# Kernel tuning notes

Hardware: AMD Instinct MI355X
Metric: run time of the kernel (lower is better)

Reference implementation:

```python
import jax, jax.numpy as jnp
import numpy as np

N, C, V, T = 16, 32, 512, 64
H, EMB, D = 4, 64, 16
OUT_C = 64
BN_EPS = 1e-5


def setup_inputs() -> dict:
    key = jax.random.key(0)
    ks = jax.random.split(key, 12)
    x = jax.random.normal(ks[0], (N, C, V, T), dtype=jnp.float32)
    t_in = jax.random.uniform(ks[1], (N, T), dtype=jnp.float32)
    # random-walk-like supports; scaled so chained nconv hops stay O(1)
    A0 = jax.random.normal(ks[2], (V, V), dtype=jnp.float32) * (V ** -0.5)
    A1 = jax.random.normal(ks[3], (V, V), dtype=jnp.float32) * (V ** -0.5)
    A2 = jax.random.normal(ks[4], (V, V), dtype=jnp.float32) * (V ** -0.5)
    factors = jax.random.normal(ks[5], (H,), dtype=jnp.float32) * 0.1
    Wq = jax.random.normal(ks[6], (H, EMB, D), dtype=jnp.float32) * (EMB ** -0.5)
    Wk = jax.random.normal(ks[7], (H, EMB, D), dtype=jnp.float32) * (EMB ** -0.5)
    GC_IN = 7 * C  # (order*support_len + 1) * in_channels
    W_out = jax.random.normal(ks[8], (OUT_C, GC_IN), dtype=jnp.float32) * (GC_IN ** -0.5)
    b_out = jnp.zeros((OUT_C,), dtype=jnp.float32)
    W_res = jax.random.normal(ks[9], (OUT_C, C), dtype=jnp.float32) * (C ** -0.5)
    b_res = jnp.zeros((OUT_C,), dtype=jnp.float32)
    bn_gamma = jnp.ones((OUT_C,), dtype=jnp.float32)
    bn_beta = jnp.zeros((OUT_C,), dtype=jnp.float32)
    bn_mean = jnp.zeros((OUT_C,), dtype=jnp.float32)
    bn_var = jnp.ones((OUT_C,), dtype=jnp.float32)
    alpha = jnp.full((1,), 0.25, dtype=jnp.float32)  # PReLU init
    return dict(x=x, t_in=t_in, A0=A0, A1=A1, A2=A2, factors=factors,
                Wq=Wq, Wk=Wk, W_out=W_out, b_out=b_out,
                W_res=W_res, b_res=b_res, bn_gamma=bn_gamma, bn_beta=bn_beta,
                bn_mean=bn_mean, bn_var=bn_var, alpha=alpha)


def reference(x, t_in, A0, A1, A2, factors, Wq, Wk, W_out, b_out,
              W_res, b_res, bn_gamma, bn_beta, bn_mean, bn_var, alpha):
    # --- learnEmbedding, all heads at once: emb[b,h,t,f] ---
    div = jnp.arange(0, EMB, 2, dtype=x.dtype)           # [EMB/2]
    div_term = jnp.exp(div[None, :] * factors[:, None])  # [H, EMB/2]
    phase = jnp.einsum('bt,hf->bhtf', t_in, div_term)    # [N,H,T,EMB/2]
    emb = jnp.concatenate([jnp.sin(phase), jnp.cos(phase)], axis=-1)  # [N,H,T,EMB]
    # --- ATT per head (t_out=None => q_emb == k_emb) ---
    q = jnp.einsum('bhtf,hfd->bhtd', emb, Wq)
    k = jnp.einsum('bhtf,hfd->bhtd', emb, Wk)
    att = jax.nn.softmax(jnp.einsum('bhtd,bhpd->bhtp', q, k) / (D ** 0.5), axis=-1)  # [N,H,T,T]
    # --- temporal mixing, summed over heads (matches per-head += loop) ---
    xt = jnp.einsum('ncvt,nhpt->ncvp', x, att)           # [N,C,V,T]
    # --- gcn: diffusion over 3 supports, order 2 ---
    outs = [xt]
    for A in (A0, A1, A2):
        x1 = jnp.einsum('ncvl,vw->ncwl', xt, A)
        x2 = jnp.einsum('ncvl,vw->ncwl', x1, A)
        outs.extend([x1, x2])
    h = jnp.concatenate(outs, axis=1)                    # [N,7C,V,T]
    # --- 1x1 output projection ---
    y = jnp.einsum('ncvt,oc->novt', h, W_out) + b_out[None, :, None, None]
    # --- residual branch: 1x1 conv + BatchNorm (eval) ---
    r = jnp.einsum('ncvt,oc->novt', x, W_res) + b_res[None, :, None, None]
    r = (r - bn_mean[None, :, None, None]) * jax.lax.rsqrt(bn_var + BN_EPS)[None, :, None, None]
    r = r * bn_gamma[None, :, None, None] + bn_beta[None, :, None, None]
    # --- residual add + PReLU (dropout is identity in eval) ---
    out = y + r
    out = jnp.where(out > 0, out, alpha[0] * out)
    return out
```

## Files before the change

kernel.cpp:

```cpp
#include <hip/hip_runtime.h>

namespace {
constexpr int N_ = 16, C_ = 32, V_ = 512, T_ = 64;
constexpr int H_ = 4, D_ = 16, OC_ = 64;
constexpr int EMB_ = 64;
constexpr int GCIN_ = 7 * C_;
constexpr int TV_ = T_ * V_;
}

typedef _Float16 f16x8 __attribute__((ext_vector_type(8)));
typedef _Float16 f16x4 __attribute__((ext_vector_type(4)));
typedef float f32x4 __attribute__((ext_vector_type(4)));

__global__ __launch_bounds__(64) void att_kernel(
    const float* __restrict__ t_in, const float* __restrict__ factors,
    const float* __restrict__ Wq, const float* __restrict__ Wk,
    float* __restrict__ att)
{
    const int n = blockIdx.x >> 2;
    const int h = blockIdx.x & 3;
    const int t = threadIdx.x;

    __shared__ float wq_l[EMB_][D_];
    __shared__ float wk_l[EMB_][D_];
    __shared__ float k_l[T_][D_ + 1];

#pragma unroll
    for (int d = 0; d < D_; ++d) {
        wq_l[t][d] = Wq[(h * EMB_ + t) * D_ + d];
        wk_l[t][d] = Wk[(h * EMB_ + t) * D_ + d];
    }
    __syncthreads();

    const float tv = t_in[n * T_ + t];
    const float fh = factors[h];
    float emb[EMB_];
#pragma unroll
    for (int j = 0; j < 32; ++j) {
        float dt = __expf((float)(2 * j) * fh);
        float ph = tv * dt;
        float s, c;
        __sincosf(ph, &s, &c);
        emb[j] = s;
        emb[j + 32] = c;
    }

    float q[D_];
#pragma unroll
    for (int d = 0; d < D_; ++d) {
        float aq = 0.f, ak = 0.f;
#pragma unroll
        for (int f = 0; f < EMB_; ++f) {
            aq += emb[f] * wq_l[f][d];
            ak += emb[f] * wk_l[f][d];
        }
        q[d] = aq;
        k_l[t][d] = ak;
    }
    __syncthreads();

    float L[T_];
    float m = -1e30f;
#pragma unroll
    for (int j = 0; j < T_; ++j) {
        float a = 0.f;
#pragma unroll
        for (int d = 0; d < D_; ++d) a += q[d] * k_l[j][d];
        a *= 0.25f;
        L[j] = a;
        m = fmaxf(m, a);
    }
    float ssum = 0.f;
#pragma unroll
    for (int j = 0; j < T_; ++j) {
        float e = __expf(L[j] - m);
        L[j] = e;
        ssum += e;
    }
    const float inv = 1.f / ssum;
    float* arow = att + (((size_t)(n * H_ + h) * T_ + t) * T_);
#pragma unroll
    for (int j = 0; j < T_; ++j) arow[j] = L[j] * inv;
}

__global__ __launch_bounds__(256) void sred_kernel(
    const float* __restrict__ att, float* __restrict__ S)
{
    int g = blockIdx.x * 256 + threadIdx.x;
    if (g >= N_ * T_ * T_) return;
    int n = g / (T_ * T_);
    int ij = g - n * (T_ * T_);
    float a = 0.f;
#pragma unroll
    for (int h = 0; h < H_; ++h) a += att[(size_t)(n * H_ + h) * (T_ * T_) + ij];
    S[g] = a;
}

__global__ __launch_bounds__(256) void prepAt_kernel(
    const float* __restrict__ A0, const float* __restrict__ A1,
    const float* __restrict__ A2, _Float16* __restrict__ At16)
{
    const int s = blockIdx.z;
    const float* A = (s == 0) ? A0 : ((s == 1) ? A1 : A2);
    const int v0 = blockIdx.y * 32, w0 = blockIdx.x * 32;
    const int tid = threadIdx.x;
    __shared__ float sT[32][33];
#pragma unroll
    for (int k = 0; k < 4; ++k) {
        int lin = k * 256 + tid;
        int i = lin >> 5, w = lin & 31;
        sT[i][w] = A[(size_t)(v0 + i) * V_ + w0 + w];
    }
    __syncthreads();
#pragma unroll
    for (int k = 0; k < 4; ++k) {
        int lin = k * 256 + tid;
        int j = lin >> 5, i = lin & 31;
        At16[(size_t)s * V_ * V_ + (size_t)(w0 + j) * V_ + v0 + i] = (_Float16)sT[i][j];
    }
}

__global__ __launch_bounds__(256) void prepxT_kernel(
    const float* __restrict__ x, _Float16* __restrict__ xT, int n0)
{
    const int b = blockIdx.z;
    const int v0 = blockIdx.x * 32;
    const int t0 = blockIdx.y * 32;
    const int tid = threadIdx.x;
    __shared__ float sT[32][33];
    const float* xb = x + ((size_t)(n0 * C_) + b) * (size_t)(V_ * T_);
    {
        int vi = tid >> 3, tq = tid & 7;
        *(float4*)&sT[vi][tq * 4] = *(const float4*)&xb[(size_t)(v0 + vi) * T_ + t0 + tq * 4];
    }
    __syncthreads();
    {
        int tj = tid >> 3, vq = tid & 7;
        f16x4 o4;
        o4[0] = (_Float16)sT[vq * 4 + 0][tj];
        o4[1] = (_Float16)sT[vq * 4 + 1][tj];
        o4[2] = (_Float16)sT[vq * 4 + 2][tj];
        o4[3] = (_Float16)sT[vq * 4 + 3][tj];
        *(f16x4*)&xT[(size_t)b * TV_ + (size_t)(t0 + tj) * V_ + v0 + vq * 4] = o4;
    }
}

__global__ __launch_bounds__(256) void prepW_kernel(
    const float* __restrict__ W_out, const float* __restrict__ b_out,
    const float* __restrict__ W_res, const float* __restrict__ b_res,
    const float* __restrict__ gamma, const float* __restrict__ beta,
    const float* __restrict__ mean, const float* __restrict__ var,
    _Float16* __restrict__ Wcat, float* __restrict__ bias)
{
    const int tid = threadIdx.x;
    const int o = tid & 63;
    const int kb = tid >> 6;
    const float rs = gamma[o] * rsqrtf(var[o] + 1e-5f);
    for (int kk = 0; kk < 64; ++kk) {
        int k = kb * 64 + kk;
        float w = (k < GCIN_) ? W_out[o * GCIN_ + k] : rs * W_res[o * C_ + (k - GCIN_)];
        Wcat[o * 256 + k] = (_Float16)w;
    }
    if (tid < 64) bias[tid] = b_out[tid] + beta[tid] + rs * (b_res[tid] - mean[tid]);
}

__global__ __launch_bounds__(256) void xtT_kernel(
    const float* __restrict__ x, const float* __restrict__ S,
    _Float16* __restrict__ XT, int n0)
{
    const int b = blockIdx.y;
    const int n = n0 + b / C_;
    const int lane = threadIdx.x & 63;
    const int wav = threadIdx.x >> 6;
    const int vbase = blockIdx.x * 256 + wav * 64;
    const int row16 = lane & 15;
    const int kg = lane >> 4;

    const float* Sn = S + (size_t)n * (T_ * T_);
    const float* xb = x + ((size_t)(n0 * C_) + b) * (V_ * T_);

    f32x4 acc[4][4];
#pragma unroll
    for (int i = 0; i < 4; ++i)
#pragma unroll
        for (int j = 0; j < 4; ++j) acc[i][j] = (f32x4){0.f, 0.f, 0.f, 0.f};

#pragma unroll
    for (int ks = 0; ks < 2; ++ks) {
        f16x8 a[4], bf[4];
#pragma unroll
        for (int mt = 0; mt < 4; ++mt) {
            const float* p = xb + (size_t)(vbase + mt * 16 + row16) * T_ + ks * 32 + kg * 8;
            float4 u = *(const float4*)p;
            float4 w = *(const float4*)(p + 4);
            f16x8 t8;
            t8[0] = (_Float16)u.x; t8[1] = (_Float16)u.y; t8[2] = (_Float16)u.z; t8[3] = (_Float16)u.w;
            t8[4] = (_Float16)w.x; t8[5] = (_Float16)w.y; t8[6] = (_Float16)w.z; t8[7] = (_Float16)w.w;
            a[mt] = t8;
        }
#pragma unroll
        for (int nt = 0; nt < 4; ++nt) {
            const float* p = Sn + (size_t)(nt * 16 + row16) * T_ + ks * 32 + kg * 8;
            float4 u = *(const float4*)p;
            float4 w = *(const float4*)(p + 4);
            f16x8 t8;
            t8[0] = (_Float16)u.x; t8[1] = (_Float16)u.y; t8[2] = (_Float16)u.z; t8[3] = (_Float16)u.w;
            t8[4] = (_Float16)w.x; t8[5] = (_Float16)w.y; t8[6] = (_Float16)w.z; t8[7] = (_Float16)w.w;
            bf[nt] = t8;
        }
#pragma unroll
        for (int nt = 0; nt < 4; ++nt)
#pragma unroll
            for (int mt = 0; mt < 4; ++mt)
                acc[mt][nt] = __builtin_amdgcn_mfma_f32_16x16x32_f16(a[mt], bf[nt], acc[mt][nt], 0, 0, 0);
    }

    _Float16* Yb = XT + (size_t)b * TV_;
#pragma unroll
    for (int mt = 0; mt < 4; ++mt)
#pragma unroll
        for (int nt = 0; nt < 4; ++nt) {
            int p = nt * 16 + row16;
            int v = vbase + mt * 16 + kg * 4;
            f16x4 h;
            h[0] = (_Float16)acc[mt][nt][0];
            h[1] = (_Float16)acc[mt][nt][1];
            h[2] = (_Float16)acc[mt][nt][2];
            h[3] = (_Float16)acc[mt][nt][3];
            *(f16x4*)&Yb[(size_t)p * V_ + v] = h;
        }
}

__global__ __launch_bounds__(512) void hopf_kernel(
    const _Float16* __restrict__ At16, _Float16* __restrict__ Hb,
    unsigned long long ASZ)
{
    const int b = blockIdx.x;
    const int s = blockIdx.y;
    const int tid = threadIdx.x;
    const int lane = tid & 63;
    const int wav = tid >> 6;
    const int wbase = wav * 64;
    const int row16 = lane & 15;
    const int kg = lane >> 4;

    __shared__ _Float16 x1s[T_ * V_];

    const _Float16* At = At16 + (size_t)s * V_ * V_;
    const _Float16* Xb = Hb + (size_t)b * TV_;
    _Float16* Y1 = Hb + (size_t)(1 + 2 * s) * ASZ + (size_t)b * TV_;
    _Float16* Y2 = Hb + (size_t)(2 + 2 * s) * ASZ + (size_t)b * TV_;

    const _Float16* ax = At + (size_t)(wbase + row16) * V_ + kg * 8;

    f32x4 acc[4][4];
    f16x8 aC[4], bC[4], aN[4], bN[4];

#pragma unroll
    for (int k = 0; k < 8; ++k) {
        int lin = k * 512 + tid;
        int t = lin >> 6;
        int v8 = (lin & 63) << 3;
        f16x8 val = *(const f16x8*)&Xb[(size_t)t * V_ + v8];
        int byte = (t * V_ + v8) * 2;
        *(f16x8*)((char*)x1s + (byte ^ ((t & 7) << 4))) = val;
    }
    __syncthreads();

#pragma unroll
    for (int i = 0; i < 4; ++i)
#pragma unroll
        for (int j = 0; j < 4; ++j) acc[i][j] = (f32x4){0.f, 0.f, 0.f, 0.f};

#pragma unroll
    for (int i = 0; i < 4; ++i) {
        aC[i] = *(const f16x8*)(ax + (size_t)i * 16 * V_);
        int t = i * 16 + row16;
        int byte = (t * V_ + kg * 8) * 2;
        bC[i] = *(const f16x8*)((const char*)x1s + (byte ^ ((t & 7) << 4)));
    }
#pragma unroll
    for (int v0 = 0; v0 < V_; v0 += 32) {
        if (v0 + 32 < V_) {
#pragma unroll
            for (int i = 0; i < 4; ++i) {
                aN[i] = *(const f16x8*)(ax + (size_t)i * 16 * V_ + v0 + 32);
                int t = i * 16 + row16;
                int byte = (t * V_ + v0 + 32 + kg * 8) * 2;
                bN[i] = *(const f16x8*)((const char*)x1s + (byte ^ ((t & 7) << 4)));
            }
        }
#pragma unroll
        for (int nt = 0; nt < 4; ++nt)
#pragma unroll
            for (int mt = 0; mt < 4; ++mt)
                acc[mt][nt] = __builtin_amdgcn_mfma_f32_16x16x32_f16(aC[mt], bC[nt], acc[mt][nt], 0, 0, 0);
#pragma unroll
        for (int i = 0; i < 4; ++i) { aC[i] = aN[i]; bC[i] = bN[i]; }
    }
    __syncthreads();

#pragma unroll
    for (int mt = 0; mt < 4; ++mt)
#pragma unroll
        for (int nt = 0; nt < 4; ++nt) {
            int t = nt * 16 + row16;
            int w = wbase + mt * 16 + kg * 4;
            f16x4 h;
            h[0] = (_Float16)acc[mt][nt][0];
            h[1] = (_Float16)acc[mt][nt][1];
            h[2] = (_Float16)acc[mt][nt][2];
            h[3] = (_Float16)acc[mt][nt][3];
            int byte = (t * V_ + w) * 2;
            *(f16x4*)((char*)x1s + (byte ^ ((t & 7) << 4))) = h;
        }
    __syncthreads();

#pragma unroll
    for (int k = 0; k < 8; ++k) {
        int lin = k * 512 + tid;
        int t = lin >> 6;
        int v8 = (lin & 63) << 3;
        int byte = (t * V_ + v8) * 2;
        f16x8 val = *(const f16x8*)((const char*)x1s + (byte ^ ((t & 7) << 4)));
        *(f16x8*)&Y1[(size_t)t * V_ + v8] = val;
    }

#pragma unroll
    for (int i = 0; i < 4; ++i)
#pragma unroll
        for (int j = 0; j < 4; ++j) acc[i][j] = (f32x4){0.f, 0.f, 0.f, 0.f};

#pragma unroll
    for (int i = 0; i < 4; ++i) {
        aC[i] = *(const f16x8*)(ax + (size_t)i * 16 * V_);
        int t = i * 16 + row16;
        int byte = (t * V_ + kg * 8) * 2;
        bC[i] = *(const f16x8*)((const char*)x1s + (byte ^ ((t & 7) << 4)));
    }
#pragma unroll
    for (int v0 = 0; v0 < V_; v0 += 32) {
        if (v0 + 32 < V_) {
#pragma unroll
            for (int i = 0; i < 4; ++i) {
                aN[i] = *(const f16x8*)(ax + (size_t)i * 16 * V_ + v0 + 32);
                int t = i * 16 + row16;
                int byte = (t * V_ + v0 + 32 + kg * 8) * 2;
                bN[i] = *(const f16x8*)((const char*)x1s + (byte ^ ((t & 7) << 4)));
            }
        }
#pragma unroll
        for (int nt = 0; nt < 4; ++nt)
#pragma unroll
            for (int mt = 0; mt < 4; ++mt)
                acc[mt][nt] = __builtin_amdgcn_mfma_f32_16x16x32_f16(aC[mt], bC[nt], acc[mt][nt], 0, 0, 0);
#pragma unroll
        for (int i = 0; i < 4; ++i) { aC[i] = aN[i]; bC[i] = bN[i]; }
    }
    __syncthreads();

#pragma unroll
    for (int mt = 0; mt < 4; ++mt)
#pragma unroll
        for (int nt = 0; nt < 4; ++nt) {
            int t = nt * 16 + row16;
            int w = wbase + mt * 16 + kg * 4;
            f16x4 h;
            h[0] = (_Float16)acc[mt][nt][0];
            h[1] = (_Float16)acc[mt][nt][1];
            h[2] = (_Float16)acc[mt][nt][2];
            h[3] = (_Float16)acc[mt][nt][3];
            int byte = (t * V_ + w) * 2;
            *(f16x4*)((char*)x1s + (byte ^ ((t & 7) << 4))) = h;
        }
    __syncthreads();

#pragma unroll
    for (int k = 0; k < 8; ++k) {
        int lin = k * 512 + tid;
        int t = lin >> 6;
        int v8 = (lin & 63) << 3;
        int byte = (t * V_ + v8) * 2;
        f16x8 val = *(const f16x8*)((const char*)x1s + (byte ^ ((t & 7) << 4)));
        *(f16x8*)&Y2[(size_t)t * V_ + v8] = val;
    }
}

__global__ __launch_bounds__(256) void epi_kernel(
    const _Float16* __restrict__ H, unsigned long long ASZ,
    const _Float16* __restrict__ Wcat, const float* __restrict__ bias,
    const float* __restrict__ alpha_p, float* __restrict__ out, int n0)
{
    const int v0 = blockIdx.x * 32;
    const int t0 = blockIdx.y * 8;
    const int nl = blockIdx.z;
    const int ng = n0 + nl;
    const int tid = threadIdx.x;
    const int lane = tid & 63;
    const int wv = tid >> 6;
    const int row16 = lane & 15;
    const int kg = lane >> 4;

    f32x4 acc[2][2][4];
#pragma unroll
    for (int j = 0; j < 2; ++j)
#pragma unroll
        for (int vs = 0; vs < 2; ++vs)
#pragma unroll
            for (int mt = 0; mt < 4; ++mt) acc[j][vs][mt] = (f32x4){0.f, 0.f, 0.f, 0.f};

    const size_t pb = ((size_t)(nl * C_ + kg * 8)) * TV_
                    + (size_t)(t0 + wv * 2) * V_ + v0 + row16;

#pragma unroll
    for (int ks = 0; ks < 8; ++ks) {
        const _Float16* Hk = H + (size_t)ks * ASZ;
        f16x8 a[4];
#pragma unroll
        for (int mt = 0; mt < 4; ++mt)
            a[mt] = *(const f16x8*)(Wcat + (mt * 16 + row16) * 256 + ks * 32 + kg * 8);
#pragma unroll
        for (int j = 0; j < 2; ++j)
#pragma unroll
            for (int vs = 0; vs < 2; ++vs) {
                const _Float16* hp = Hk + pb + (size_t)j * V_ + vs * 16;
                f16x8 bf;
#pragma unroll
                for (int e = 0; e < 8; ++e) bf[e] = hp[(size_t)e * TV_];
#pragma unroll
                for (int mt = 0; mt < 4; ++mt)
                    acc[j][vs][mt] = __builtin_amdgcn_mfma_f32_16x16x32_f16(a[mt], bf, acc[j][vs][mt], 0, 0, 0);
            }
    }

    __shared__ float sC[16 * 33 * 9];
    const float al = alpha_p[0];
    const int ot = tid >> 4;
    const int vvt = tid & 15;

    for (int mt = 0; mt < 4; ++mt) {
#pragma unroll
        for (int j = 0; j < 2; ++j)
#pragma unroll
            for (int vs = 0; vs < 2; ++vs)
#pragma unroll
                for (int r = 0; r < 4; ++r)
                    sC[((kg * 4 + r) * 33 + vs * 16 + row16) * 9 + wv * 2 + j] = acc[j][vs][mt][r];
        __syncthreads();
        const float bo = bias[mt * 16 + ot];
#pragma unroll
        for (int vh = 0; vh < 2; ++vh) {
            const int vl = vvt + vh * 16;
            float vals[8];
#pragma unroll
            for (int tt = 0; tt < 8; ++tt) {
                float u = sC[(ot * 33 + vl) * 9 + tt] + bo;
                vals[tt] = u > 0.f ? u : al * u;
            }
            float* op = out + (((size_t)ng * OC_ + mt * 16 + ot) * V_ + v0 + vl) * T_ + t0;
            *(float4*)&op[0] = make_float4(vals[0], vals[1], vals[2], vals[3]);
            *(float4*)&op[4] = make_float4(vals[4], vals[5], vals[6], vals[7]);
        }
        __syncthreads();
    }
}

extern "C" void kernel_launch(void* const* d_in, const int* in_sizes, int n_in,
                              void* d_out, int out_size, void* d_ws, size_t ws_size,
                              hipStream_t stream)
{
    const float* x       = (const float*)d_in[0];
    const float* t_in    = (const float*)d_in[1];
    const float* A0      = (const float*)d_in[2];
    const float* A1      = (const float*)d_in[3];
    const float* A2      = (const float*)d_in[4];
    const float* factors = (const float*)d_in[5];
    const float* Wq      = (const float*)d_in[6];
    const float* Wk      = (const float*)d_in[7];
    const float* W_out   = (const float*)d_in[8];
    const float* b_out   = (const float*)d_in[9];
    const float* W_res   = (const float*)d_in[10];
    const float* b_res   = (const float*)d_in[11];
    const float* gamma   = (const float*)d_in[12];
    const float* beta    = (const float*)d_in[13];
    const float* mean    = (const float*)d_in[14];
    const float* var     = (const float*)d_in[15];
    const float* alpha   = (const float*)d_in[16];
    float* out = (float*)d_out;

    float* att = (float*)d_ws;
    float* S    = att + (size_t)N_ * H_ * T_ * T_;
    float* bias = S + (size_t)N_ * T_ * T_;
    _Float16* At16 = (_Float16*)(bias + 64);
    _Float16* Wcat = At16 + (size_t)3 * V_ * V_;
    _Float16* Hbase = Wcat + (size_t)64 * 256;

    const size_t fixed = ((size_t)N_ * H_ * T_ * T_ + (size_t)N_ * T_ * T_ + 64) * 4
                       + ((size_t)3 * V_ * V_ + 64 * 256) * 2;
    int Nc = 16;
    while (Nc > 1 && fixed + (size_t)8 * Nc * C_ * T_ * V_ * 2 > ws_size) Nc >>= 1;
    const size_t ASZ = (size_t)Nc * C_ * T_ * V_;

    att_kernel<<<N_ * H_, 64, 0, stream>>>(t_in, factors, Wq, Wk, att);
    sred_kernel<<<(N_ * T_ * T_ + 255) / 256, 256, 0, stream>>>(att, S);
    prepAt_kernel<<<dim3(16, 16, 3), 256, 0, stream>>>(A0, A1, A2, At16);
    prepW_kernel<<<1, 256, 0, stream>>>(W_out, b_out, W_res, b_res,
                                        gamma, beta, mean, var, Wcat, bias);

    for (int n0 = 0; n0 < N_; n0 += Nc) {
        const int nsl = Nc * C_;
        xtT_kernel<<<dim3(2, nsl), 256, 0, stream>>>(x, S, Hbase, n0);
        prepxT_kernel<<<dim3(16, 2, nsl), 256, 0, stream>>>(x, Hbase + (size_t)7 * ASZ, n0);
        hopf_kernel<<<dim3(nsl, 3), 512, 0, stream>>>(At16, Hbase, (unsigned long long)ASZ);
        epi_kernel<<<dim3(16, 8, Nc), 256, 0, stream>>>(
            Hbase, (unsigned long long)ASZ, Wcat, bias, alpha, out, n0);
    }
}
```

Measured before the change: 497.8 us.

## Process two slices per hop block to reuse A-matrix fragment loads

Each hopf block now handles two (n,c) slices at once. It keeps both 64x512 fp16 slices in LDS (128 KB) and applies every loaded A-fragment to two accumulator sets, which halves the global A traffic per slice and the grid size. In exchange it doubles the accumulator registers, lowering occupancy and the overlap between blocks. The LDS B-fragment loads are no longer prefetched one step ahead.

Result: faster. 484.9 us (-2.6%).

```diff
diff --git a/kernel.cpp b/kernel.cpp
--- a/kernel.cpp
+++ b/kernel.cpp
@@ -235,7 +235,7 @@
     const _Float16* __restrict__ At16, _Float16* __restrict__ Hb,
     unsigned long long ASZ)
 {
-    const int b = blockIdx.x;
+    const int bp = blockIdx.x;
     const int s = blockIdx.y;
     const int tid = threadIdx.x;
     const int lane = tid & 63;
@@ -244,77 +244,22 @@
     const int row16 = lane & 15;
     const int kg = lane >> 4;
 
-    __shared__ _Float16 x1s[T_ * V_];
+    __shared__ _Float16 xs0[T_ * V_];
+    __shared__ _Float16 xs1[T_ * V_];
 
     const _Float16* At = At16 + (size_t)s * V_ * V_;
-    const _Float16* Xb = Hb + (size_t)b * TV_;
-    _Float16* Y1 = Hb + (size_t)(1 + 2 * s) * ASZ + (size_t)b * TV_;
-    _Float16* Y2 = Hb + (size_t)(2 + 2 * s) * ASZ + (size_t)b * TV_;
+    const int b0 = bp * 2;
+    const _Float16* Xb0 = Hb + (size_t)b0 * TV_;
+    const _Float16* Xb1 = Hb + (size_t)(b0 + 1) * TV_;
+    _Float16* Y1a = Hb + (size_t)(1 + 2 * s) * ASZ + (size_t)b0 * TV_;
+    _Float16* Y1b = Y1a + TV_;
+    _Float16* Y2a = Hb + (size_t)(2 + 2 * s) * ASZ + (size_t)b0 * TV_;
+    _Float16* Y2b = Y2a + TV_;
 
     const _Float16* ax = At + (size_t)(wbase + row16) * V_ + kg * 8;
 
-    f32x4 acc[4][4];
-    f16x8 aC[4], bC[4], aN[4], bN[4];
-
-#pragma unroll
-    for (int k = 0; k < 8; ++k) {
-        int lin = k * 512 + tid;
-        int t = lin >> 6;
-        int v8 = (lin & 63) << 3;
-        f16x8 val = *(const f16x8*)&Xb[(size_t)t * V_ + v8];
-        int byte = (t * V_ + v8) * 2;
-        *(f16x8*)((char*)x1s + (byte ^ ((t & 7) << 4))) = val;
-    }
-    __syncthreads();
-
-#pragma unroll
-    for (int i = 0; i < 4; ++i)
-#pragma unroll
-        for (int j = 0; j < 4; ++j) acc[i][j] = (f32x4){0.f, 0.f, 0.f, 0.f};
-
-#pragma unroll
-    for (int i = 0; i < 4; ++i) {
-        aC[i] = *(const f16x8*)(ax + (size_t)i * 16 * V_);
-        int t = i * 16 + row16;
-        int byte = (t * V_ + kg * 8) * 2;
-        bC[i] = *(const f16x8*)((const char*)x1s + (byte ^ ((t & 7) << 4)));
-    }
-#pragma unroll
-    for (int v0 = 0; v0 < V_; v0 += 32) {
-        if (v0 + 32 < V_) {
-#pragma unroll
-            for (int i = 0; i < 4; ++i) {
-                aN[i] = *(const f16x8*)(ax + (size_t)i * 16 * V_ + v0 + 32);
-                int t = i * 16 + row16;
-                int byte = (t * V_ + v0 + 32 + kg * 8) * 2;
-                bN[i] = *(const f16x8*)((const char*)x1s + (byte ^ ((t & 7) << 4)));
-            }
-        }
-#pragma unroll
-        for (int nt = 0; nt < 4; ++nt)
-#pragma unroll
-            for (int mt = 0; mt < 4; ++mt)
-                acc[mt][nt] = __builtin_amdgcn_mfma_f32_16x16x32_f16(aC[mt], bC[nt], acc[mt][nt], 0, 0, 0);
-#pragma unroll
-        for (int i = 0; i < 4; ++i) { aC[i] = aN[i]; bC[i] = bN[i]; }
-    }
-    __syncthreads();
-
-#pragma unroll
-    for (int mt = 0; mt < 4; ++mt)
-#pragma unroll
-        for (int nt = 0; nt < 4; ++nt) {
-            int t = nt * 16 + row16;
-            int w = wbase + mt * 16 + kg * 4;
-            f16x4 h;
-            h[0] = (_Float16)acc[mt][nt][0];
-            h[1] = (_Float16)acc[mt][nt][1];
-            h[2] = (_Float16)acc[mt][nt][2];
-            h[3] = (_Float16)acc[mt][nt][3];
-            int byte = (t * V_ + w) * 2;
-            *(f16x4*)((char*)x1s + (byte ^ ((t & 7) << 4))) = h;
-        }
-    __syncthreads();
+    f32x4 acc0[4][4], acc1[4][4];
+    f16x8 aC[4], aN[4];
 
 #pragma unroll
     for (int k = 0; k < 8; ++k) {
@@ -322,40 +267,49 @@
         int t = lin >> 6;
         int v8 = (lin & 63) << 3;
         int byte = (t * V_ + v8) * 2;
-        f16x8 val = *(const f16x8*)((const char*)x1s + (byte ^ ((t & 7) << 4)));
-        *(f16x8*)&Y1[(size_t)t * V_ + v8] = val;
-    }
+        f16x8 v0v = *(const f16x8*)&Xb0[(size_t)t * V_ + v8];
+        f16x8 v1v = *(const f16x8*)&Xb1[(size_t)t * V_ + v8];
+        *(f16x8*)((char*)xs0 + (byte ^ ((t & 7) << 4))) = v0v;
+        *(f16x8*)((char*)xs1 + (byte ^ ((t & 7) << 4))) = v1v;
+    }
+    __syncthreads();
 
 #pragma unroll
     for (int i = 0; i < 4; ++i)
 #pragma unroll
-        for (int j = 0; j < 4; ++j) acc[i][j] = (f32x4){0.f, 0.f, 0.f, 0.f};
-
-#pragma unroll
-    for (int i = 0; i < 4; ++i) {
+        for (int j = 0; j < 4; ++j) {
+            acc0[i][j] = (f32x4){0.f, 0.f, 0.f, 0.f};
+            acc1[i][j] = (f32x4){0.f, 0.f, 0.f, 0.f};
+        }
+#pragma unroll
+    for (int i = 0; i < 4; ++i)
         aC[i] = *(const f16x8*)(ax + (size_t)i * 16 * V_);
-        int t = i * 16 + row16;
-        int byte = (t * V_ + kg * 8) * 2;
-        bC[i] = *(const f16x8*)((const char*)x1s + (byte ^ ((t & 7) << 4)));
-    }
-#pragma unroll
-    for (int v0 = 0; v0 < V_; v0 += 32) {
-        if (v0 + 32 < V_) {
-#pragma unroll
-            for (int i = 0; i < 4; ++i) {
+
+#pragma unroll
+    for (int it = 0; it < 16; ++it) {
+        const int v0 = it * 32;
+        if (it < 15) {
+#pragma unroll
+            for (int i = 0; i < 4; ++i)
                 aN[i] = *(const f16x8*)(ax + (size_t)i * 16 * V_ + v0 + 32);
-                int t = i * 16 + row16;
-                int byte = (t * V_ + v0 + 32 + kg * 8) * 2;
-                bN[i] = *(const f16x8*)((const char*)x1s + (byte ^ ((t & 7) << 4)));
+        }
+        f16x8 b0v[4], b1v[4];
+#pragma unroll
+        for (int nt = 0; nt < 4; ++nt) {
+            int t = nt * 16 + row16;
+            int byte = (t * V_ + v0 + kg * 8) * 2;
+            b0v[nt] = *(const f16x8*)((const char*)xs0 + (byte ^ ((t & 7) << 4)));
+            b1v[nt] = *(const f16x8*)((const char*)xs1 + (byte ^ ((t & 7) << 4)));
+        }
+#pragma unroll
+        for (int nt = 0; nt < 4; ++nt)
+#pragma unroll
+            for (int mt = 0; mt < 4; ++mt) {
+                acc0[mt][nt] = __builtin_amdgcn_mfma_f32_16x16x32_f16(aC[mt], b0v[nt], acc0[mt][nt], 0, 0, 0);
+                acc1[mt][nt] = __builtin_amdgcn_mfma_f32_16x16x32_f16(aC[mt], b1v[nt], acc1[mt][nt], 0, 0, 0);
             }
-        }
-#pragma unroll
-        for (int nt = 0; nt < 4; ++nt)
-#pragma unroll
-            for (int mt = 0; mt < 4; ++mt)
-                acc[mt][nt] = __builtin_amdgcn_mfma_f32_16x16x32_f16(aC[mt], bC[nt], acc[mt][nt], 0, 0, 0);
-#pragma unroll
-        for (int i = 0; i < 4; ++i) { aC[i] = aN[i]; bC[i] = bN[i]; }
+#pragma unroll
+        for (int i = 0; i < 4; ++i) aC[i] = aN[i];
     }
     __syncthreads();
 
@@ -365,13 +319,14 @@
         for (int nt = 0; nt < 4; ++nt) {
             int t = nt * 16 + row16;
             int w = wbase + mt * 16 + kg * 4;
-            f16x4 h;
-            h[0] = (_Float16)acc[mt][nt][0];
-            h[1] = (_Float16)acc[mt][nt][1];
-            h[2] = (_Float16)acc[mt][nt][2];
-            h[3] = (_Float16)acc[mt][nt][3];
             int byte = (t * V_ + w) * 2;
-            *(f16x4*)((char*)x1s + (byte ^ ((t & 7) << 4))) = h;
+            f16x4 h0, h1;
+            h0[0] = (_Float16)acc0[mt][nt][0]; h0[1] = (_Float16)acc0[mt][nt][1];
+            h0[2] = (_Float16)acc0[mt][nt][2]; h0[3] = (_Float16)acc0[mt][nt][3];
+            h1[0] = (_Float16)acc1[mt][nt][0]; h1[1] = (_Float16)acc1[mt][nt][1];
+            h1[2] = (_Float16)acc1[mt][nt][2]; h1[3] = (_Float16)acc1[mt][nt][3];
+            *(f16x4*)((char*)xs0 + (byte ^ ((t & 7) << 4))) = h0;
+            *(f16x4*)((char*)xs1 + (byte ^ ((t & 7) << 4))) = h1;
         }
     __syncthreads();
 
@@ -381,8 +336,78 @@
         int t = lin >> 6;
         int v8 = (lin & 63) << 3;
         int byte = (t * V_ + v8) * 2;
-        f16x8 val = *(const f16x8*)((const char*)x1s + (byte ^ ((t & 7) << 4)));
-        *(f16x8*)&Y2[(size_t)t * V_ + v8] = val;
+        f16x8 v0v = *(const f16x8*)((const char*)xs0 + (byte ^ ((t & 7) << 4)));
+        f16x8 v1v = *(const f16x8*)((const char*)xs1 + (byte ^ ((t & 7) << 4)));
+        *(f16x8*)&Y1a[(size_t)t * V_ + v8] = v0v;
+        *(f16x8*)&Y1b[(size_t)t * V_ + v8] = v1v;
+    }
+
+#pragma unroll
+    for (int i = 0; i < 4; ++i)
+#pragma unroll
+        for (int j = 0; j < 4; ++j) {
+            acc0[i][j] = (f32x4){0.f, 0.f, 0.f, 0.f};
+            acc1[i][j] = (f32x4){0.f, 0.f, 0.f, 0.f};
+        }
+#pragma unroll
+    for (int i = 0; i < 4; ++i)
+        aC[i] = *(const f16x8*)(ax + (size_t)i * 16 * V_);
+
+#pragma unroll
+    for (int it = 0; it < 16; ++it) {
+        const int v0 = it * 32;
+        if (it < 15) {
+#pragma unroll
+            for (int i = 0; i < 4; ++i)
+                aN[i] = *(const f16x8*)(ax + (size_t)i * 16 * V_ + v0 + 32);
+        }
+        f16x8 b0v[4], b1v[4];
+#pragma unroll
+        for (int nt = 0; nt < 4; ++nt) {
+            int t = nt * 16 + row16;
+            int byte = (t * V_ + v0 + kg * 8) * 2;
+            b0v[nt] = *(const f16x8*)((const char*)xs0 + (byte ^ ((t & 7) << 4)));
+            b1v[nt] = *(const f16x8*)((const char*)xs1 + (byte ^ ((t & 7) << 4)));
+        }
+#pragma unroll
+        for (int nt = 0; nt < 4; ++nt)
+#pragma unroll
+            for (int mt = 0; mt < 4; ++mt) {
+                acc0[mt][nt] = __builtin_amdgcn_mfma_f32_16x16x32_f16(aC[mt], b0v[nt], acc0[mt][nt], 0, 0, 0);
+                acc1[mt][nt] = __builtin_amdgcn_mfma_f32_16x16x32_f16(aC[mt], b1v[nt], acc1[mt][nt], 0, 0, 0);
+            }
+#pragma unroll
+        for (int i = 0; i < 4; ++i) aC[i] = aN[i];
+    }
+    __syncthreads();
+
+#pragma unroll
+    for (int mt = 0; mt < 4; ++mt)
+#pragma unroll
+        for (int nt = 0; nt < 4; ++nt) {
+            int t = nt * 16 + row16;
+            int w = wbase + mt * 16 + kg * 4;
+            int byte = (t * V_ + w) * 2;
+            f16x4 h0, h1;
+            h0[0] = (_Float16)acc0[mt][nt][0]; h0[1] = (_Float16)acc0[mt][nt][1];
+            h0[2] = (_Float16)acc0[mt][nt][2]; h0[3] = (_Float16)acc0[mt][nt][3];
+            h1[0] = (_Float16)acc1[mt][nt][0]; h1[1] = (_Float16)acc1[mt][nt][1];
+            h1[2] = (_Float16)acc1[mt][nt][2]; h1[3] = (_Float16)acc1[mt][nt][3];
+            *(f16x4*)((char*)xs0 + (byte ^ ((t & 7) << 4))) = h0;
+            *(f16x4*)((char*)xs1 + (byte ^ ((t & 7) << 4))) = h1;
+        }
+    __syncthreads();
+
+#pragma unroll
+    for (int k = 0; k < 8; ++k) {
+        int lin = k * 512 + tid;
+        int t = lin >> 6;
+        int v8 = (lin & 63) << 3;
+        int byte = (t * V_ + v8) * 2;
+        f16x8 v0v = *(const f16x8*)((const char*)xs0 + (byte ^ ((t & 7) << 4)));
+        f16x8 v1v = *(const f16x8*)((const char*)xs1 + (byte ^ ((t & 7) << 4)));
+        *(f16x8*)&Y2a[(size_t)t * V_ + v8] = v0v;
+        *(f16x8*)&Y2b[(size_t)t * V_ + v8] = v1v;
     }
 }
 
@@ -511,7 +536,7 @@
         const int nsl = Nc * C_;
         xtT_kernel<<<dim3(2, nsl), 256, 0, stream>>>(x, S, Hbase, n0);
         prepxT_kernel<<<dim3(16, 2, nsl), 256, 0, stream>>>(x, Hbase + (size_t)7 * ASZ, n0);
-        hopf_kernel<<<dim3(nsl, 3), 512, 0, stream>>>(At16, Hbase, (unsigned long long)ASZ);
+        hopf_kernel<<<dim3(nsl / 2, 3), 512, 0, stream>>>(At16, Hbase, (unsigned long long)ASZ);
         epi_kernel<<<dim3(16, 8, Nc), 256, 0, stream>>>(
             Hbase, (unsigned long long)ASZ, Wcat, bias, alpha, out, n0);
     }
```
